# Optimization experiments

Measured on AMD Instinct MI355X. Metric: run time of the kernel, lower is better.

## Reference

```python
import jax, jax.numpy as jnp
import numpy as np

B, T, C, H = 2, 2048, 2048, 16
HD = C // H


def setup_inputs() -> dict:
    key = jax.random.key(0)
    ks = jax.random.split(key, 5)
    s = 0.02  # init scale for weights
    return {
        "x": jax.random.normal(ks[0], (B, T, C), jnp.float32),
        "Wq": jax.random.normal(ks[1], (C, C), jnp.float32) * s,
        "Wk": jax.random.normal(ks[2], (C, C), jnp.float32) * s,
        "Wv": jax.random.normal(ks[3], (C, C), jnp.float32) * s,
        "Wo": jax.random.normal(ks[4], (C, C), jnp.float32) * s,
        "bo": jnp.zeros((C,), jnp.float32),
    }


def _alibi_slopes(n_head):
    # power-of-2 path of _get_alibi_slopes (n_head=16 is a power of 2)
    return jnp.array([1.0 / 2 ** (i + 1) for i in range(n_head)], jnp.float32)


def reference(x, Wq, Wk, Wv, Wo, bo):
    b, t, c = x.shape
    h, hd = H, HD
    scale = 1.0 / np.sqrt(hd)
    # nn.Linear (no bias): y = x @ W.T; split heads -> (B,H,T,HD)
    q = (x @ Wq.T).reshape(b, t, h, hd).transpose(0, 2, 1, 3)
    k = (x @ Wk.T).reshape(b, t, h, hd).transpose(0, 2, 1, 3)
    v = (x @ Wv.T).reshape(b, t, h, hd).transpose(0, 2, 1, 3)
    scores = jnp.einsum("bhtd,bhsd->bhts", q, k) * scale  # (B,H,T,T)
    pos = jnp.arange(t)
    diff = pos[:, None] - pos[None, :]  # (T,T), i-j
    slopes = _alibi_slopes(h)
    bias = slopes[:, None, None] * diff.astype(jnp.float32)  # (H,T,T)
    causal = diff >= 0  # lower-triangular mask
    bias = jnp.where(causal[None, :, :], bias, -jnp.inf)
    scores = scores + bias[None]  # (B,H,T,T)
    attn = jax.nn.softmax(scores, axis=-1)  # dropout = identity (eval mode)
    out = jnp.einsum("bhts,bhsd->bhtd", attn, v)
    out = out.transpose(0, 2, 1, 3).reshape(b, t, c)
    out = out @ Wo.T + bo  # proj_dropout = identity (eval mode)
    return out, attn
```

## Files before the change

### kernel.cpp

```cpp
#include <hip/hip_runtime.h>
#include <hip/hip_bf16.h>

#define DEVINL __device__ __forceinline__

typedef __attribute__((ext_vector_type(8))) short bf16x8;
typedef __attribute__((ext_vector_type(4))) float f32x4;

DEVINL ushort f2bf(float f) {
  unsigned u = __float_as_uint(f);
  u += 0x7fffu + ((u >> 16) & 1u);
  return (ushort)(u >> 16);
}

DEVINL void gl_lds16(const void* g, void* lds) {
  __builtin_amdgcn_global_load_lds(
      (const __attribute__((address_space(1))) void*)g,
      (__attribute__((address_space(3))) void*)lds, 16, 0, 0);
}

DEVINL f32x4 mfma16(bf16x8 a, bf16x8 b, f32x4 c) {
  return __builtin_amdgcn_mfma_f32_16x16x32_bf16(a, b, c, 0, 0, 0);
}

__global__ __launch_bounds__(256) void cast_all_kernel(const float4* __restrict__ x,
                                                       const float4* __restrict__ wq,
                                                       const float4* __restrict__ wk,
                                                       const float4* __restrict__ wv,
                                                       const float4* __restrict__ wo,
                                                       ushort4* __restrict__ xb,
                                                       ushort4* __restrict__ wqb,
                                                       ushort4* __restrict__ wkb,
                                                       ushort4* __restrict__ wvb,
                                                       ushort4* __restrict__ wob) {
  const int blk = (int)blockIdx.x;
  const float4* src;
  ushort4* dst;
  int base;
  if (blk < 2048)      { src = x;  dst = xb;  base = blk; }
  else if (blk < 3072) { src = wq; dst = wqb; base = blk - 2048; }
  else if (blk < 4096) { src = wk; dst = wkb; base = blk - 3072; }
  else if (blk < 5120) { src = wv; dst = wvb; base = blk - 4096; }
  else                 { src = wo; dst = wob; base = blk - 5120; }
  const int idx0 = base * 1024 + (int)threadIdx.x;
#pragma unroll
  for (int i = 0; i < 4; ++i) {
    const int idx = idx0 + i * 256;
    float4 v = src[idx];
    dst[idx] = make_ushort4(f2bf(v.x), f2bf(v.y), f2bf(v.z), f2bf(v.w));
  }
}

template <int MODE>
__global__ __launch_bounds__(256) void gemm_nt(const ushort* __restrict__ A,
                                               const ushort* __restrict__ Bm,
                                               ushort* __restrict__ Qo,
                                               ushort* __restrict__ Ko,
                                               ushort* __restrict__ Vo,
                                               float* __restrict__ Fo,
                                               const float* __restrict__ bias,
                                               int M, int N, int K) {
  __shared__ __align__(16) ushort Al[2][8192];
  __shared__ __align__(16) ushort Bl[2][8192];
  const int tid = (int)threadIdx.x;
  const int l = tid & 63, w = tid >> 6;
  const int wr = w >> 1, wc = w & 1;
  const int lr = l & 15, lg = l >> 4;

  const int nwg = (int)(gridDim.x * gridDim.y);
  const int flat = (int)(blockIdx.y * gridDim.x + blockIdx.x);
  const int swz = (flat & 7) * (nwg >> 3) + (flat >> 3);
  const int bx = swz % (int)gridDim.x, by = swz / (int)gridDim.x;
  const int rowT = by * 128, colT = bx * 128;

  f32x4 acc[4][4] = {};

  auto stage = [&](int kt, int buf) {
#pragma unroll
    for (int q = 0; q < 4; ++q) {
      int s = q * 256 + tid;
      int rb = s >> 7, ks = (s >> 6) & 1, sl = s & 63;
      size_t koff = (size_t)(kt + ks * 32 + (sl >> 4) * 8);
      gl_lds16(A + (size_t)(rowT + rb * 16 + (sl & 15)) * K + koff,
               &Al[buf][(size_t)(q * 256 + (tid & 192)) * 8]);
      gl_lds16(Bm + (size_t)(colT + rb * 16 + (sl & 15)) * K + koff,
               &Bl[buf][(size_t)(q * 256 + (tid & 192)) * 8]);
    }
  };

  stage(0, 0);
  __syncthreads();
  int cur = 0;
  for (int kt = 0; kt < K; kt += 64) {
    if (kt + 64 < K) stage(kt + 64, cur ^ 1);
#pragma unroll
    for (int ks = 0; ks < 2; ++ks) {
      bf16x8 af[4], bfv[4];
#pragma unroll
      for (int i = 0; i < 4; ++i) {
        af[i]  = *(const bf16x8*)(&Al[cur][(((wr * 4 + i) * 2 + ks) * 64 + l) * 8]);
        bfv[i] = *(const bf16x8*)(&Bl[cur][(((wc * 4 + i) * 2 + ks) * 64 + l) * 8]);
      }
#pragma unroll
      for (int i = 0; i < 4; ++i)
#pragma unroll
        for (int j = 0; j < 4; ++j)
          acc[i][j] = mfma16(af[i], bfv[j], acc[i][j]);
    }
    __syncthreads();
    cur ^= 1;
  }

  const int seg = colT >> 11;
#pragma unroll
  for (int i = 0; i < 4; ++i) {
#pragma unroll
    for (int j = 0; j < 4; ++j) {
      const int col = colT + wc * 64 + j * 16 + lr;
#pragma unroll
      for (int e = 0; e < 4; ++e) {
        const int row = rowT + wr * 64 + i * 16 + lg * 4 + e;
        float v = acc[i][j][e];
        if (MODE == 3) {
          const int c = col & 2047;
          if (seg == 0)      Qo[(size_t)row * 2048 + c] = f2bf(v);
          else if (seg == 1) Ko[(size_t)row * 2048 + c] = f2bf(v);
          else               Vo[((size_t)((row >> 11) * 2048 + c)) * 2048 + (row & 2047)] = f2bf(v);
        } else {
          Fo[(size_t)row * 2048 + col] = v + bias[col];
        }
      }
    }
  }
}

__global__ __launch_bounds__(512) void flash_kernel(const ushort* __restrict__ Qg,
                                                    const ushort* __restrict__ Kg,
                                                    const ushort* __restrict__ Vt,
                                                    ushort* __restrict__ Og,
                                                    float2* __restrict__ stats) {
  __shared__ __align__(16) ushort Kl[2][8192];
  __shared__ __align__(16) ushort Vl[2][8192];
  __shared__ __align__(16) ushort Pl[8][1024];

  const int flat = (int)(blockIdx.y * gridDim.x + blockIdx.x);
  const int swz = (flat & 7) * 64 + (flat >> 3);
  const int bx = swz & 15, bh = swz >> 4;
  const int b = bh >> 4, h = bh & 15;
  const int tid = (int)threadIdx.x, l = tid & 63, w = tid >> 6;
  const int lr = l & 15, lg = l >> 4;
  const float scale = 0.08838834764831845f;
  const float slope = exp2f(-(float)(h + 1));
  const ushort* Kbase = Kg + ((size_t)b * 2048) * 2048 + h * 128;
  const ushort* Vbase = Vt + ((size_t)b * 2048 + h * 128) * 2048;

  auto stage = [&](int jt, int buf) {
#pragma unroll
    for (int q = 0; q < 2; ++q) {
      const int s = q * 512 + tid;
      const int sl = s & 63;
      const int cb = s >> 8, ks = (s >> 6) & 3;
      gl_lds16(Kbase + (size_t)(jt * 64 + cb * 16 + (sl & 15)) * 2048 + ks * 32 + (sl >> 4) * 8,
               &Kl[buf][(size_t)(q * 512 + (tid & 448)) * 8]);
      const int db = s >> 7, k2 = (s >> 6) & 1;
      gl_lds16(Vbase + (size_t)(db * 16 + (sl & 15)) * 2048 + jt * 64 + k2 * 32 + (sl >> 4) * 8,
               &Vl[buf][(size_t)(q * 512 + (tid & 448)) * 8]);
    }
  };

  for (int half = 0; half < 2; ++half) {
    const int q128 = (half == 0) ? 15 - bx : bx;
    const int qr0 = q128 * 128 + w * 16;
    const int jtmax = 2 * q128 + 1;

    bf16x8 qf[4];
#pragma unroll
    for (int ks = 0; ks < 4; ++ks)
      qf[ks] = *(const bf16x8*)(Qg + ((size_t)b * 2048 + qr0 + lr) * 2048 + h * 128 + ks * 32 + lg * 8);

    float runmax[4], runsum[4];
    f32x4 o[8] = {};
#pragma unroll
    for (int j = 0; j < 4; ++j) { runmax[j] = -1e30f; runsum[j] = 0.f; }

    stage(jtmax, 0);
    __syncthreads();

    for (int jt = jtmax; jt >= 0; --jt) {
      const int cur = (jtmax - jt) & 1;
      if (jt > 0) stage(jt - 1, cur ^ 1);

      if (qr0 + 15 >= jt * 64) {
        f32x4 sc[4];
        __builtin_amdgcn_s_setprio(1);
#pragma unroll
        for (int cb = 0; cb < 4; ++cb) {
          f32x4 a = {};
#pragma unroll
          for (int ks = 0; ks < 4; ++ks) {
            bf16x8 kf = *(const bf16x8*)(&Kl[cur][((cb * 4 + ks) * 64 + l) * 8]);
            a = mfma16(qf[ks], kf, a);
          }
          sc[cb] = a;
        }
        __builtin_amdgcn_s_setprio(0);
#pragma unroll
        for (int cb = 0; cb < 4; ++cb) {
          const int kj = jt * 64 + cb * 16 + lr;
#pragma unroll
          for (int j = 0; j < 4; ++j) {
            const int qi = qr0 + lg * 4 + j;
            sc[cb][j] = (kj <= qi) ? sc[cb][j] * scale + slope * (float)(qi - kj) : -__builtin_inff();
          }
        }

        float ml[4];
        bool grow = false;
#pragma unroll
        for (int j = 0; j < 4; ++j) {
          ml[j] = fmaxf(fmaxf(sc[0][j], sc[1][j]), fmaxf(sc[2][j], sc[3][j]));
          grow = grow || (ml[j] > runmax[j]);
        }
        if (__any(grow)) {
#pragma unroll
          for (int j = 0; j < 4; ++j) {
            float m = ml[j];
#pragma unroll
            for (int d = 1; d < 16; d <<= 1) m = fmaxf(m, __shfl_xor(m, d));
            const float nm = fmaxf(runmax[j], m);
            const float f = __expf(runmax[j] - nm);
            runsum[j] *= f;
#pragma unroll
            for (int db = 0; db < 8; ++db) o[db][j] *= f;
            runmax[j] = nm;
          }
        }

#pragma unroll
        for (int cb = 0; cb < 4; ++cb) {
          const int kc = cb * 16 + lr;
#pragma unroll
          for (int j = 0; j < 4; ++j) {
            const float p = __expf(sc[cb][j] - runmax[j]);
            runsum[j] += p;
            const int l2 = (((kc & 31) >> 3) << 4) | (lg * 4 + j);
            Pl[w][((kc >> 5) * 64 + l2) * 8 + (kc & 7)] = f2bf(p);
          }
        }

        bf16x8 pf0 = *(const bf16x8*)(&Pl[w][(size_t)l * 8]);
        bf16x8 pf1 = *(const bf16x8*)(&Pl[w][(size_t)(64 + l) * 8]);
        __builtin_amdgcn_s_setprio(1);
#pragma unroll
        for (int db = 0; db < 8; ++db) {
          o[db] = mfma16(pf0, *(const bf16x8*)(&Vl[cur][((db * 2 + 0) * 64 + l) * 8]), o[db]);
          o[db] = mfma16(pf1, *(const bf16x8*)(&Vl[cur][((db * 2 + 1) * 64 + l) * 8]), o[db]);
        }
        __builtin_amdgcn_s_setprio(0);
      }
      __syncthreads();
    }

#pragma unroll
    for (int j = 0; j < 4; ++j) {
      float s = runsum[j];
#pragma unroll
      for (int d = 1; d < 16; d <<= 1) s += __shfl_xor(s, d);
      const float iv = 1.0f / s;
      if (lr == 0) stats[(size_t)bh * 2048 + qr0 + lg * 4 + j] = make_float2(runmax[j], iv);
#pragma unroll
      for (int db = 0; db < 8; ++db) o[db][j] *= iv;
    }
#pragma unroll
    for (int db = 0; db < 8; ++db)
#pragma unroll
      for (int j = 0; j < 4; ++j)
        Og[((size_t)b * 2048 + qr0 + lg * 4 + j) * 2048 + h * 128 + db * 16 + lr] = f2bf(o[db][j]);
  }
}

__global__ __launch_bounds__(256) void probs_kernel(const ushort* __restrict__ Qg,
                                                    const ushort* __restrict__ Kg,
                                                    const float2* __restrict__ stats,
                                                    float* __restrict__ attn_out) {
  const int kb = (int)blockIdx.x, qb = (int)blockIdx.y, bh = (int)blockIdx.z;
  const int tid = (int)threadIdx.x;

  if (kb > qb) {
    float* base = attn_out + ((size_t)bh * 2048 + qb * 128) * 2048 + kb * 128;
    const f32x4 z = {0.f, 0.f, 0.f, 0.f};
#pragma unroll
    for (int it = 0; it < 16; ++it) {
      const int idx = it * 256 + tid;
      __builtin_nontemporal_store(z, (f32x4*)(base + (size_t)(idx >> 5) * 2048 + (idx & 31) * 4));
    }
    return;
  }

  __shared__ __align__(16) ushort Ql[16384];
  __shared__ __align__(16) ushort Kl[16384];
  const int b = bh >> 4, h = bh & 15;
  const int l = tid & 63, w = tid >> 6;
  const int wr = w >> 1, wc = w & 1;
  const int lr = l & 15, lg = l >> 4;
  const float scale = 0.08838834764831845f;
  const float slope = exp2f(-(float)(h + 1));

#pragma unroll
  for (int q = 0; q < 8; ++q) {
    const int s = q * 256 + tid;
    const int sl = s & 63, rb = s >> 8, ks = (s >> 6) & 3;
    const size_t koff = (size_t)(h * 128 + ks * 32 + (sl >> 4) * 8);
    gl_lds16(Qg + ((size_t)b * 2048 + qb * 128 + rb * 16 + (sl & 15)) * 2048 + koff,
             Ql + (size_t)(q * 256 + (tid & 192)) * 8);
    gl_lds16(Kg + ((size_t)b * 2048 + kb * 128 + rb * 16 + (sl & 15)) * 2048 + koff,
             Kl + (size_t)(q * 256 + (tid & 192)) * 8);
  }
  __syncthreads();

  f32x4 acc[4][4] = {};
#pragma unroll
  for (int ks = 0; ks < 4; ++ks) {
    bf16x8 af[4], bfv[4];
#pragma unroll
    for (int i = 0; i < 4; ++i) {
      af[i]  = *(const bf16x8*)(Ql + (((wr * 4 + i) * 4 + ks) * 64 + l) * 8);
      bfv[i] = *(const bf16x8*)(Kl + (((wc * 4 + i) * 4 + ks) * 64 + l) * 8);
    }
#pragma unroll
    for (int i = 0; i < 4; ++i)
#pragma unroll
      for (int j = 0; j < 4; ++j)
        acc[i][j] = mfma16(af[i], bfv[j], acc[i][j]);
  }

  float2 st[4][4];
#pragma unroll
  for (int i = 0; i < 4; ++i)
#pragma unroll
    for (int e = 0; e < 4; ++e)
      st[i][e] = stats[(size_t)bh * 2048 + qb * 128 + wr * 64 + i * 16 + lg * 4 + e];

#pragma unroll
  for (int i = 0; i < 4; ++i) {
#pragma unroll
    for (int j = 0; j < 4; ++j) {
      const int kj = kb * 128 + wc * 64 + j * 16 + lr;
#pragma unroll
      for (int e = 0; e < 4; ++e) {
        const int qi = qb * 128 + wr * 64 + i * 16 + lg * 4 + e;
        const float sv = acc[i][j][e] * scale + slope * (float)(qi - kj);
        float p = __expf(sv - st[i][e].x) * st[i][e].y;
        if (kj > qi) p = 0.f;
        __builtin_nontemporal_store(p, &attn_out[((size_t)bh * 2048 + qi) * 2048 + kj]);
      }
    }
  }
}

extern "C" void kernel_launch(void* const* d_in, const int* in_sizes, int n_in,
                              void* d_out, int out_size, void* d_ws, size_t ws_size,
                              hipStream_t stream) {
  (void)in_sizes; (void)n_in; (void)out_size; (void)ws_size;
  const float* x  = (const float*)d_in[0];
  const float* Wq = (const float*)d_in[1];
  const float* Wk = (const float*)d_in[2];
  const float* Wv = (const float*)d_in[3];
  const float* Wo = (const float*)d_in[4];
  const float* bo = (const float*)d_in[5];

  float* outp  = (float*)d_out;
  float* attnp = outp + (size_t)4096 * 2048;

  char* ws = (char*)d_ws;
  ushort* xb   = (ushort*)(ws);
  ushort* wqkv = (ushort*)(ws + (16ull << 20));
  ushort* wob  = (ushort*)(ws + (40ull << 20));
  ushort* Qb   = (ushort*)(ws + (48ull << 20));
  ushort* Kb   = (ushort*)(ws + (64ull << 20));
  ushort* Vtb  = (ushort*)(ws + (80ull << 20));
  ushort* Ob   = (ushort*)(ws + (96ull << 20));
  float2* stats = (float2*)(ws);

  cast_all_kernel<<<6144, 256, 0, stream>>>(
      (const float4*)x, (const float4*)Wq, (const float4*)Wk, (const float4*)Wv,
      (const float4*)Wo, (ushort4*)xb, (ushort4*)wqkv, (ushort4*)(wqkv + 4194304),
      (ushort4*)(wqkv + 2 * 4194304), (ushort4*)wob);

  gemm_nt<3><<<dim3(48, 32), 256, 0, stream>>>(xb, wqkv, Qb, Kb, Vtb, nullptr, nullptr,
                                               4096, 6144, 2048);

  flash_kernel<<<dim3(16, 32), 512, 0, stream>>>(Qb, Kb, Vtb, Ob, stats);
  probs_kernel<<<dim3(16, 16, 32), 256, 0, stream>>>(Qb, Kb, stats, attnp);

  gemm_nt<2><<<dim3(16, 32), 256, 0, stream>>>(Ob, wob, nullptr, nullptr, nullptr, outp, bo,
                                               4096, 2048, 2048);
}
```

Measured before the change: 615.5 us.

## Shrink flash query tile to 64 rows with 4 waves and nontemporal output stores

```diff
diff --git a/kernel.cpp b/kernel.cpp
--- a/kernel.cpp
+++ b/kernel.cpp
@@ -126,21 +126,21 @@
           else if (seg == 1) Ko[(size_t)row * 2048 + c] = f2bf(v);
           else               Vo[((size_t)((row >> 11) * 2048 + c)) * 2048 + (row & 2047)] = f2bf(v);
         } else {
-          Fo[(size_t)row * 2048 + col] = v + bias[col];
-        }
-      }
-    }
-  }
-}
-
-__global__ __launch_bounds__(512) void flash_kernel(const ushort* __restrict__ Qg,
+          __builtin_nontemporal_store(v + bias[col], &Fo[(size_t)row * 2048 + col]);
+        }
+      }
+    }
+  }
+}
+
+__global__ __launch_bounds__(256) void flash_kernel(const ushort* __restrict__ Qg,
                                                     const ushort* __restrict__ Kg,
                                                     const ushort* __restrict__ Vt,
                                                     ushort* __restrict__ Og,
                                                     float2* __restrict__ stats) {
   __shared__ __align__(16) ushort Kl[2][8192];
   __shared__ __align__(16) ushort Vl[2][8192];
-  __shared__ __align__(16) ushort Pl[8][1024];
+  __shared__ __align__(16) ushort Pl[4][1024];
 
   const int flat = (int)(blockIdx.y * gridDim.x + blockIdx.x);
   const int swz = (flat & 7) * 64 + (flat >> 3);
@@ -153,24 +153,9 @@
   const ushort* Kbase = Kg + ((size_t)b * 2048) * 2048 + h * 128;
   const ushort* Vbase = Vt + ((size_t)b * 2048 + h * 128) * 2048;
 
-  auto stage = [&](int jt, int buf) {
-#pragma unroll
-    for (int q = 0; q < 2; ++q) {
-      const int s = q * 512 + tid;
-      const int sl = s & 63;
-      const int cb = s >> 8, ks = (s >> 6) & 3;
-      gl_lds16(Kbase + (size_t)(jt * 64 + cb * 16 + (sl & 15)) * 2048 + ks * 32 + (sl >> 4) * 8,
-               &Kl[buf][(size_t)(q * 512 + (tid & 448)) * 8]);
-      const int db = s >> 7, k2 = (s >> 6) & 1;
-      gl_lds16(Vbase + (size_t)(db * 16 + (sl & 15)) * 2048 + jt * 64 + k2 * 32 + (sl >> 4) * 8,
-               &Vl[buf][(size_t)(q * 512 + (tid & 448)) * 8]);
-    }
-  };
-
   for (int half = 0; half < 2; ++half) {
-    const int q128 = (half == 0) ? 15 - bx : bx;
-    const int qr0 = q128 * 128 + w * 16;
-    const int jtmax = 2 * q128 + 1;
+    const int qb = (half == 0) ? 31 - bx : bx;
+    const int qr0 = qb * 64 + w * 16;
 
     bf16x8 qf[4];
 #pragma unroll
@@ -180,83 +165,94 @@
     float runmax[4], runsum[4];
     f32x4 o[8] = {};
 #pragma unroll
-    for (int j = 0; j < 4; ++j) { runmax[j] = -1e30f; runsum[j] = 0.f; }
-
-    stage(jtmax, 0);
+    for (int j = 0; j < 4; ++j) { runmax[j] = -__builtin_inff(); runsum[j] = 0.f; }
+
+    auto stage = [&](int jt, int buf) {
+#pragma unroll
+      for (int q = 0; q < 4; ++q) {
+        const int s = q * 256 + tid;
+        const int sl = s & 63;
+        const int cb = s >> 8, ks = (s >> 6) & 3;
+        gl_lds16(Kbase + (size_t)(jt * 64 + cb * 16 + (sl & 15)) * 2048 + ks * 32 + (sl >> 4) * 8,
+                 &Kl[buf][(size_t)(q * 256 + (tid & 192)) * 8]);
+        const int db = s >> 7, k2 = (s >> 6) & 1;
+        gl_lds16(Vbase + (size_t)(db * 16 + (sl & 15)) * 2048 + jt * 64 + k2 * 32 + (sl >> 4) * 8,
+                 &Vl[buf][(size_t)(q * 256 + (tid & 192)) * 8]);
+      }
+    };
+
+    stage(qb, 0);
     __syncthreads();
 
-    for (int jt = jtmax; jt >= 0; --jt) {
-      const int cur = (jtmax - jt) & 1;
+    for (int jt = qb; jt >= 0; --jt) {
+      const int cur = (qb - jt) & 1;
       if (jt > 0) stage(jt - 1, cur ^ 1);
 
-      if (qr0 + 15 >= jt * 64) {
-        f32x4 sc[4];
-        __builtin_amdgcn_s_setprio(1);
-#pragma unroll
-        for (int cb = 0; cb < 4; ++cb) {
-          f32x4 a = {};
-#pragma unroll
-          for (int ks = 0; ks < 4; ++ks) {
-            bf16x8 kf = *(const bf16x8*)(&Kl[cur][((cb * 4 + ks) * 64 + l) * 8]);
-            a = mfma16(qf[ks], kf, a);
-          }
-          sc[cb] = a;
-        }
-        __builtin_amdgcn_s_setprio(0);
-#pragma unroll
-        for (int cb = 0; cb < 4; ++cb) {
-          const int kj = jt * 64 + cb * 16 + lr;
-#pragma unroll
-          for (int j = 0; j < 4; ++j) {
-            const int qi = qr0 + lg * 4 + j;
-            sc[cb][j] = (kj <= qi) ? sc[cb][j] * scale + slope * (float)(qi - kj) : -__builtin_inff();
-          }
-        }
-
-        float ml[4];
-        bool grow = false;
+      f32x4 sc[4];
+      __builtin_amdgcn_s_setprio(1);
+#pragma unroll
+      for (int cb = 0; cb < 4; ++cb) {
+        f32x4 a = {};
+#pragma unroll
+        for (int ks = 0; ks < 4; ++ks) {
+          bf16x8 kf = *(const bf16x8*)(&Kl[cur][((cb * 4 + ks) * 64 + l) * 8]);
+          a = mfma16(qf[ks], kf, a);
+        }
+        sc[cb] = a;
+      }
+      __builtin_amdgcn_s_setprio(0);
+#pragma unroll
+      for (int cb = 0; cb < 4; ++cb) {
+        const int kj = jt * 64 + cb * 16 + lr;
 #pragma unroll
         for (int j = 0; j < 4; ++j) {
-          ml[j] = fmaxf(fmaxf(sc[0][j], sc[1][j]), fmaxf(sc[2][j], sc[3][j]));
-          grow = grow || (ml[j] > runmax[j]);
-        }
-        if (__any(grow)) {
-#pragma unroll
-          for (int j = 0; j < 4; ++j) {
-            float m = ml[j];
-#pragma unroll
-            for (int d = 1; d < 16; d <<= 1) m = fmaxf(m, __shfl_xor(m, d));
-            const float nm = fmaxf(runmax[j], m);
-            const float f = __expf(runmax[j] - nm);
-            runsum[j] *= f;
-#pragma unroll
-            for (int db = 0; db < 8; ++db) o[db][j] *= f;
-            runmax[j] = nm;
-          }
-        }
-
-#pragma unroll
-        for (int cb = 0; cb < 4; ++cb) {
-          const int kc = cb * 16 + lr;
-#pragma unroll
-          for (int j = 0; j < 4; ++j) {
-            const float p = __expf(sc[cb][j] - runmax[j]);
-            runsum[j] += p;
-            const int l2 = (((kc & 31) >> 3) << 4) | (lg * 4 + j);
-            Pl[w][((kc >> 5) * 64 + l2) * 8 + (kc & 7)] = f2bf(p);
-          }
-        }
-
-        bf16x8 pf0 = *(const bf16x8*)(&Pl[w][(size_t)l * 8]);
-        bf16x8 pf1 = *(const bf16x8*)(&Pl[w][(size_t)(64 + l) * 8]);
-        __builtin_amdgcn_s_setprio(1);
-#pragma unroll
-        for (int db = 0; db < 8; ++db) {
-          o[db] = mfma16(pf0, *(const bf16x8*)(&Vl[cur][((db * 2 + 0) * 64 + l) * 8]), o[db]);
-          o[db] = mfma16(pf1, *(const bf16x8*)(&Vl[cur][((db * 2 + 1) * 64 + l) * 8]), o[db]);
-        }
-        __builtin_amdgcn_s_setprio(0);
-      }
+          const int qi = qr0 + lg * 4 + j;
+          sc[cb][j] = (kj <= qi) ? sc[cb][j] * scale + slope * (float)(qi - kj) : -__builtin_inff();
+        }
+      }
+
+      float nm[4];
+      bool need = false;
+#pragma unroll
+      for (int j = 0; j < 4; ++j) {
+        float m = fmaxf(fmaxf(sc[0][j], sc[1][j]), fmaxf(sc[2][j], sc[3][j]));
+#pragma unroll
+        for (int d = 1; d < 16; d <<= 1) m = fmaxf(m, __shfl_xor(m, d));
+        nm[j] = fmaxf(runmax[j], m);
+        need = need || (nm[j] > runmax[j]);
+      }
+      if (__any(need)) {
+#pragma unroll
+        for (int j = 0; j < 4; ++j) {
+          const float f = __expf(runmax[j] - nm[j]);
+          runsum[j] *= f;
+#pragma unroll
+          for (int db = 0; db < 8; ++db) o[db][j] *= f;
+          runmax[j] = nm[j];
+        }
+      }
+
+#pragma unroll
+      for (int cb = 0; cb < 4; ++cb) {
+        const int kc = cb * 16 + lr;
+#pragma unroll
+        for (int j = 0; j < 4; ++j) {
+          const float p = __expf(sc[cb][j] - runmax[j]);
+          runsum[j] += p;
+          const int l2 = (((kc & 31) >> 3) << 4) | (lg * 4 + j);
+          Pl[w][((kc >> 5) * 64 + l2) * 8 + (kc & 7)] = f2bf(p);
+        }
+      }
+
+      bf16x8 pf0 = *(const bf16x8*)(&Pl[w][(size_t)l * 8]);
+      bf16x8 pf1 = *(const bf16x8*)(&Pl[w][(size_t)(64 + l) * 8]);
+      __builtin_amdgcn_s_setprio(1);
+#pragma unroll
+      for (int db = 0; db < 8; ++db) {
+        o[db] = mfma16(pf0, *(const bf16x8*)(&Vl[cur][((db * 2 + 0) * 64 + l) * 8]), o[db]);
+        o[db] = mfma16(pf1, *(const bf16x8*)(&Vl[cur][((db * 2 + 1) * 64 + l) * 8]), o[db]);
+      }
+      __builtin_amdgcn_s_setprio(0);
       __syncthreads();
     }
 
@@ -389,7 +385,7 @@
   gemm_nt<3><<<dim3(48, 32), 256, 0, stream>>>(xb, wqkv, Qb, Kb, Vtb, nullptr, nullptr,
                                                4096, 6144, 2048);
 
-  flash_kernel<<<dim3(16, 32), 512, 0, stream>>>(Qb, Kb, Vtb, Ob, stats);
+  flash_kernel<<<dim3(16, 32), 256, 0, stream>>>(Qb, Kb, Vtb, Ob, stats);
   probs_kernel<<<dim3(16, 16, 32), 256, 0, stream>>>(Qb, Kb, stats, attnp);
 
   gemm_nt<2><<<dim3(16, 32), 256, 0, stream>>>(Ob, wob, nullptr, nullptr, nullptr, outp, bo,
```

New measurement: 523.6 us. -14.9%, faster.
